# Kernel optimization log

Hardware: AMD Instinct MI355X
Metric: run time of the kernel (lower is better)

## Reference

```python
import jax, jax.numpy as jnp
import numpy as np

G, NPG, C, H, F, L = 256, 128, 16, 128, 128, 3
N = G * NPG          # 32768 nodes
E = 524288           # 16 edges per node on average
REG, REG_C = 0.01, 0.01
LN_EPS = 1e-5


def setup_inputs() -> dict:
    key = jax.random.key(0)
    ks = jax.random.split(key, 20)
    x = jax.random.normal(ks[0], (N, F), dtype=jnp.float32)
    # edges kept within each graph so dense pooling matches to_dense_batch semantics
    epg = E // G
    offs = jnp.repeat(jnp.arange(G, dtype=jnp.int64) * NPG, epg)
    src = jax.random.randint(ks[1], (E,), 0, NPG, dtype=jnp.int64) + offs
    tgt = jax.random.randint(ks[2], (E,), 0, NPG, dtype=jnp.int64) + offs
    edge_index = jnp.stack([src, tgt])
    mask_breaks = jax.random.bernoulli(ks[3], 0.5, (E,))
    s = jax.random.uniform(ks[4], (N, C), dtype=jnp.float32)
    batch = jnp.repeat(jnp.arange(G, dtype=jnp.int64), NPG)
    sc = 1.0 / np.sqrt(H)
    Wn = jax.random.normal(ks[5], (L, H, H), dtype=jnp.float32) * sc
    bn_ = jax.random.normal(ks[6], (L, H), dtype=jnp.float32) * sc
    Wo = jax.random.normal(ks[7], (L, H, H), dtype=jnp.float32) * sc
    bo = jax.random.normal(ks[8], (L, H), dtype=jnp.float32) * sc
    Wr = jax.random.normal(ks[9], (L, H, H), dtype=jnp.float32) * sc
    ln_g = jnp.ones((L, H), dtype=jnp.float32)
    ln_b = jnp.zeros((L, H), dtype=jnp.float32)
    fln_g = jnp.ones((H,), dtype=jnp.float32)
    fln_b = jnp.zeros((H,), dtype=jnp.float32)
    lin_w = jax.random.normal(ks[10], (1, H), dtype=jnp.float32) * sc
    bias = jnp.zeros((1,), dtype=jnp.float32)
    return {"x": x, "edge_index": edge_index, "mask_breaks": mask_breaks, "s": s,
            "batch": batch, "Wn": Wn, "bn_": bn_, "Wo": Wo, "bo": bo, "Wr": Wr,
            "ln_g": ln_g, "ln_b": ln_b, "fln_g": fln_g, "fln_b": fln_b,
            "lin_w": lin_w, "bias": bias}


def _layernorm(h, g, b):
    mu = jnp.mean(h, axis=-1, keepdims=True)
    v = jnp.mean(jnp.square(h - mu), axis=-1, keepdims=True)
    return (h - mu) * jax.lax.rsqrt(v + LN_EPS) * g + b


def reference(x, edge_index, mask_breaks, s, batch, Wn, bn_, Wo, bo, Wr,
              ln_g, ln_b, fln_g, fln_b, lin_w, bias):
    src, tgt = edge_index[0], edge_index[1]
    ones_e = jnp.ones((E,), dtype=x.dtype)
    cnt = jax.ops.segment_sum(ones_e, tgt, num_segments=N)          # in-degree
    inv_cnt = (1.0 / jnp.maximum(cnt, 1.0))[:, None]
    h = x
    for i in range(L):
        x_in = h @ Wn[i].T + bn_[i]
        x_out = h @ Wo[i].T + bo[i]
        x_root = h @ Wr[i].T
        msg = jnp.where(mask_breaks[:, None], x_in[src], x_out[src])  # [E,H]
        agg = jax.ops.segment_sum(msg, tgt, num_segments=N) * inv_cnt  # mean aggr
        h = jax.nn.relu(_layernorm(agg + x_root, ln_g[i], ln_b[i]))
    # dense per-graph views (equal-size graphs, batch ids sorted -> reshape)
    xd = h.reshape(G, NPG, H)
    sd = s.reshape(G, NPG, C)
    pooled = jnp.einsum("gnc,gnh->gch", sd, xd)                      # [G,C,H]
    pooled = _layernorm(pooled, fln_g, fln_b)
    xc = pooled @ lin_w.T                                            # [G,C,1]
    col_sum = sd.sum(axis=1)                                          # [G,C]
    cmask = (col_sum > 0)[..., None]
    xc = xc * cmask.astype(xc.dtype)
    out = xc.sum(axis=1) + bias                                      # [G,1]
    reg_loss = jnp.abs(Wo).sum() + jnp.abs(bo).sum()
    denom = (cmask.astype(xc.dtype).squeeze(-1) + 1e-7).sum(axis=1, keepdims=True)
    l1_loss = (jnp.abs(xc).sum(axis=1) / denom).mean()
    losses = REG * reg_loss + REG_C * l1_loss
    return out, losses, xc
```

## Files before the change

kernel.cpp:

```cpp
#include <hip/hip_runtime.h>

#define NN   32768
#define HD   128
#define EE   524288
#define GG   256
#define EPG  2048
#define CCd  16
#define LLd  3

typedef short short8 __attribute__((ext_vector_type(8)));
typedef float f32x4 __attribute__((ext_vector_type(4)));

__device__ __forceinline__ unsigned short f2bf(float f) {
  unsigned u = __builtin_bit_cast(unsigned, f);
  return (unsigned short)((u + 0x7FFFu + ((u >> 16) & 1u)) >> 16);
}
__device__ __forceinline__ unsigned bfpack(float a, float b) {
  return (unsigned)f2bf(a) | ((unsigned)f2bf(b) << 16);
}

__device__ __forceinline__ int hchunk(int f, int c) {
  return f * 128 + (((c & 8) | ((c ^ f ^ (f >> 3)) & 7)) << 3);
}
__device__ __forceinline__ int hidx(int f, int t) {
  return hchunk(f, t >> 3) + (t & 7);
}

__global__ __launch_bounds__(256) void convert_w_kernel(const float* __restrict__ Wn, const float* __restrict__ Wo,
                                                        const float* __restrict__ Wr, const float* __restrict__ bo,
                                                        unsigned* __restrict__ Wnb, unsigned* __restrict__ Wob,
                                                        unsigned* __restrict__ Wrb, float* __restrict__ wsreg) {
  int i = blockIdx.x * 256 + threadIdx.x;
  float4 a = *(const float4*)(Wn + (size_t)i * 4);
  float4 b = *(const float4*)(Wo + (size_t)i * 4);
  float4 c = *(const float4*)(Wr + (size_t)i * 4);
  *(uint2*)(Wnb + (size_t)i * 2) = make_uint2(bfpack(a.x, a.y), bfpack(a.z, a.w));
  *(uint2*)(Wob + (size_t)i * 2) = make_uint2(bfpack(b.x, b.y), bfpack(b.z, b.w));
  *(uint2*)(Wrb + (size_t)i * 2) = make_uint2(bfpack(c.x, c.y), bfpack(c.z, c.w));
  float s = fabsf(b.x) + fabsf(b.y) + fabsf(b.z) + fabsf(b.w);
  if (blockIdx.x == 0 && threadIdx.x < 96) {
    float4 d = *(const float4*)(bo + threadIdx.x * 4);
    s += fabsf(d.x) + fabsf(d.y) + fabsf(d.z) + fabsf(d.w);
  }
#pragma unroll
  for (int mk = 1; mk < 64; mk <<= 1) s += __shfl_xor(s, mk, 64);
  if ((threadIdx.x & 63) == 0) atomicAdd(wsreg, s);
}

__global__ __launch_bounds__(512) void fused_kernel(
    const float* __restrict__ x,
    const int* __restrict__ esrc, const int* __restrict__ etgt, const int* __restrict__ emask,
    const unsigned short* __restrict__ Wnb, const unsigned short* __restrict__ Wob,
    const unsigned short* __restrict__ Wrb,
    const float* __restrict__ bn, const float* __restrict__ bo,
    const float* __restrict__ lng, const float* __restrict__ lnb,
    const float* __restrict__ s,
    const float* __restrict__ flng, const float* __restrict__ flnb,
    const float* __restrict__ linw, const float* __restrict__ bias,
    float* __restrict__ out, float* __restrict__ l1g) {
  __shared__ __align__(16) unsigned short hTs[128 * 128];
  __shared__ __align__(16) unsigned short sTs[16 * 136];
  __shared__ __align__(16) unsigned Mlds[2 * 128 * 64];
  __shared__ __align__(16) unsigned Wlds[128 * 64];
  __shared__ float finS[128], foutS[128];
  __shared__ float colsumS[CCd], xcs[CCd], axcs[CCd], msk[CCd];

  const int g = blockIdx.x;
  const int tid = threadIdx.x;
  const int wave = tid >> 6;
  const int lane = tid & 63;
  const int m = lane & 15;
  const int q = lane >> 4;
  const int t0 = wave << 4;

  unsigned* const slotB = Mlds;
  unsigned* const slotC = Mlds + 8192;

  auto w_stage = [&](const unsigned short* __restrict__ Wg, unsigned* slot) {
#pragma unroll
    for (int c = 0; c < 4; ++c) {
      int row = c * 32 + wave * 4 + (lane >> 4);
      int lc = (lane & 15) ^ (row & 7);
      const unsigned short* gp = Wg + row * 128 + lc * 8;
      unsigned* lp = slot + c * 2048 + wave * 256;
      __builtin_amdgcn_global_load_lds(
          (const __attribute__((address_space(1))) unsigned*)gp,
          (__attribute__((address_space(3))) unsigned*)lp, 16, 0, 0);
    }
  };
  auto wfrag = [&](const unsigned* slot, int ct, int ksg) -> short8 {
    return *(const short8*)&slot[(ct * 16 + m) * 64 + (((ksg * 4 + q) ^ (m & 7)) << 2)];
  };

  w_stage(Wnb, Wlds);
  int et[4], es[4], em[4];
  {
    const int e0 = g * EPG;
#pragma unroll
    for (int i = 0; i < 4; ++i) {
      int e = e0 + i * 512 + tid;
      et[i] = etgt[e]; es[i] = esrc[e]; em[i] = emask[e];
    }
  }

  {
    uint4* cz = (uint4*)Mlds;
#pragma unroll
    for (int i = 0; i < 8; ++i) cz[i * 512 + tid] = make_uint4(0u, 0u, 0u, 0u);

    const float4* xg = (const float4*)(x + (size_t)g * 16384);
#pragma unroll
    for (int i = 0; i < 8; ++i) {
      int flat = i * 512 + tid;
      int t = flat >> 5, f0 = (flat & 31) << 2;
      float4 v = xg[flat];
      hTs[hidx(f0 + 0, t)] = f2bf(v.x);
      hTs[hidx(f0 + 1, t)] = f2bf(v.y);
      hTs[hidx(f0 + 2, t)] = f2bf(v.z);
      hTs[hidx(f0 + 3, t)] = f2bf(v.w);
    }
    {
      int t = tid >> 2, c0 = (tid & 3) << 2;
      float4 v = *(const float4*)(s + (size_t)g * 2048 + t * 16 + c0);
      sTs[(c0 + 0) * 136 + t] = f2bf(v.x);
      sTs[(c0 + 1) * 136 + t] = f2bf(v.y);
      sTs[(c0 + 2) * 136 + t] = f2bf(v.z);
      sTs[(c0 + 3) * 136 + t] = f2bf(v.w);
    }
    if (tid < 64) {
      int c = tid & 15, qq = tid >> 4;
      float cs = 0.f;
      for (int tt = qq; tt < 128; tt += 4) cs += s[(size_t)g * 2048 + tt * 16 + c];
      cs += __shfl_xor(cs, 16); cs += __shfl_xor(cs, 32);
      if (qq == 0) colsumS[c] = cs;
    }
  }
  __syncthreads();

  {
#pragma unroll
    for (int i = 0; i < 4; ++i) {
      int t = et[i] & 127;
      int sl = es[i] & 127;
      int dir = (em[i] != 0) ? 0 : 1;
      atomicAdd(&Mlds[dir * 8192 + t * 64 + (((sl >> 3) ^ (t & 7)) << 2) + ((sl >> 1) & 3)],
                1u << ((sl & 1) * 16));
    }
  }
  __syncthreads();

  short8 mfr[2][4];
  {
    const int t = t0 + m;
    const int mm = m & 7;
    unsigned nin = 0, nout = 0;
#pragma unroll
    for (int k4 = 0; k4 < 4; ++k4) {
      int sl = (((q * 4 + k4) ^ mm) & 15) << 2;
      uint4 a = *(const uint4*)&Mlds[t * 64 + sl];
      uint4 b = *(const uint4*)&Mlds[8192 + t * 64 + sl];
      nin  += (a.x & 0xffffu) + (a.x >> 16) + (a.y & 0xffffu) + (a.y >> 16)
            + (a.z & 0xffffu) + (a.z >> 16) + (a.w & 0xffffu) + (a.w >> 16);
      nout += (b.x & 0xffffu) + (b.x >> 16) + (b.y & 0xffffu) + (b.y >> 16)
            + (b.z & 0xffffu) + (b.z >> 16) + (b.w & 0xffffu) + (b.w >> 16);
    }
    nin  += __shfl_xor((int)nin, 16);  nin  += __shfl_xor((int)nin, 32);
    nout += __shfl_xor((int)nout, 16); nout += __shfl_xor((int)nout, 32);
    unsigned dg = nin + nout;
    float inv = 1.0f / (float)(dg > 0 ? dg : 1);
    if (q == 0) { finS[t] = (float)nin * inv; foutS[t] = (float)nout * inv; }
#pragma unroll
    for (int d = 0; d < 2; ++d)
#pragma unroll
      for (int ksg = 0; ksg < 4; ++ksg) {
        int sl = (((ksg * 4 + q) ^ mm) & 15) << 2;
        uint4 v = *(const uint4*)&Mlds[d * 8192 + t * 64 + sl];
        uint4 o;
        o.x = bfpack((float)(v.x & 0xffffu) * inv, (float)(v.x >> 16) * inv);
        o.y = bfpack((float)(v.y & 0xffffu) * inv, (float)(v.y >> 16) * inv);
        o.z = bfpack((float)(v.z & 0xffffu) * inv, (float)(v.z >> 16) * inv);
        o.w = bfpack((float)(v.w & 0xffffu) * inv, (float)(v.w >> 16) * inv);
        mfr[d][ksg] = __builtin_bit_cast(short8, o);
      }
  }
  __syncthreads();

  w_stage(Wob, slotB);
  w_stage(Wrb, slotC);
  __syncthreads();

  for (int L = 0; L < LLd; ++L) {
    const bool more = (L < LLd - 1);
    f32x4 pre[8];
#pragma unroll
    for (int ct = 0; ct < 8; ++ct) pre[ct] = (f32x4){0.f, 0.f, 0.f, 0.f};

#pragma unroll
    for (int sg = 0; sg < 2; ++sg) {
      const unsigned* slot = (sg == 0) ? (const unsigned*)Wlds : (const unsigned*)slotB;
#pragma unroll
      for (int kso = 0; kso < 4; ++kso) {
        f32x4 acc0 = (f32x4){0.f, 0.f, 0.f, 0.f};
        f32x4 acc1 = (f32x4){0.f, 0.f, 0.f, 0.f};
#pragma unroll
        for (int ksi = 0; ksi < 4; ++ksi) {
          short8 bfr = mfr[sg][ksi];
          short8 a0 = *(const short8*)&hTs[hchunk((2 * kso) * 16 + m, ksi * 4 + q)];
          acc0 = __builtin_amdgcn_mfma_f32_16x16x32_bf16(a0, bfr, acc0, 0, 0, 0);
          short8 a1 = *(const short8*)&hTs[hchunk((2 * kso + 1) * 16 + m, ksi * 4 + q)];
          acc1 = __builtin_amdgcn_mfma_f32_16x16x32_bf16(a1, bfr, acc1, 0, 0, 0);
        }
        unsigned pk[4];
#pragma unroll
        for (int r = 0; r < 4; ++r) pk[r] = bfpack(acc0[r], acc1[r]);
        short8 afr;
#pragma unroll
        for (int j = 0; j < 8; ++j) {
          int srcl = ((((q & 1) << 1) + (j >> 2)) << 4) + m;
          unsigned v = (unsigned)__shfl((int)pk[j & 3], srcl, 64);
          afr[j] = (short)(unsigned short)((q >> 1) ? (v >> 16) : (v & 0xffffu));
        }
#pragma unroll
        for (int ct = 0; ct < 8; ++ct) {
          short8 bfr = wfrag(slot, ct, kso);
          pre[ct] = __builtin_amdgcn_mfma_f32_16x16x32_bf16(afr, bfr, pre[ct], 0, 0, 0);
        }
      }
    }
#pragma unroll
    for (int hf = 0; hf < 2; ++hf)
#pragma unroll
      for (int ksl = 0; ksl < 2; ++ksl) {
        const int ksg = hf * 2 + ksl;
        short8 afr;
#pragma unroll
        for (int j = 0; j < 8; ++j)
          afr[j] = (short)hTs[hidx(ksg * 32 + q * 8 + j, t0 + m)];
#pragma unroll
        for (int ct = 0; ct < 8; ++ct) {
          short8 bfr = wfrag(slotC, ct, ksg);
          pre[ct] = __builtin_amdgcn_mfma_f32_16x16x32_bf16(afr, bfr, pre[ct], 0, 0, 0);
        }
      }
    __syncthreads();
    if (more) {
      w_stage(Wnb + (L + 1) * 16384, Wlds);
      w_stage(Wob + (L + 1) * 16384, slotB);
      w_stage(Wrb + (L + 1) * 16384, slotC);
    }
    {
      float fiv[4], fov[4];
#pragma unroll
      for (int r = 0; r < 4; ++r) { fiv[r] = finS[t0 + q * 4 + r]; fov[r] = foutS[t0 + q * 4 + r]; }
#pragma unroll
      for (int ct2 = 0; ct2 < 8; ct2 += 4) {
        float bn4[4], bo4[4];
#pragma unroll
        for (int cc = 0; cc < 4; ++cc) {
          int c = L * 128 + (ct2 + cc) * 16 + m;
          bn4[cc] = bn[c]; bo4[cc] = bo[c];
        }
#pragma unroll
        for (int cc = 0; cc < 4; ++cc)
#pragma unroll
          for (int r = 0; r < 4; ++r)
            pre[ct2 + cc][r] += fiv[r] * bn4[cc] + fov[r] * bo4[cc];
      }
      float gv[8], bv[8];
#pragma unroll
      for (int ct = 0; ct < 8; ++ct) {
        int c = L * 128 + ct * 16 + m;
        gv[ct] = lng[c]; bv[ct] = lnb[c];
      }
#pragma unroll
      for (int r = 0; r < 4; ++r) {
        const int tl = q * 4 + r;
        float sum = 0.f;
#pragma unroll
        for (int ct = 0; ct < 8; ++ct) sum += pre[ct][r];
        sum += __shfl_xor(sum, 1); sum += __shfl_xor(sum, 2);
        sum += __shfl_xor(sum, 4); sum += __shfl_xor(sum, 8);
        const float mu = sum * (1.0f / 128.0f);
        float sq = 0.f;
#pragma unroll
        for (int ct = 0; ct < 8; ++ct) { float d = pre[ct][r] - mu; sq += d * d; }
        sq += __shfl_xor(sq, 1); sq += __shfl_xor(sq, 2);
        sq += __shfl_xor(sq, 4); sq += __shfl_xor(sq, 8);
        const float rstd = rsqrtf(sq * (1.0f / 128.0f) + 1e-5f);
#pragma unroll
        for (int ct = 0; ct < 8; ++ct) {
          float o = fmaxf((pre[ct][r] - mu) * rstd * gv[ct] + bv[ct], 0.0f);
          hTs[hidx(ct * 16 + m, t0 + tl)] = f2bf(o);
        }
      }
    }
    __syncthreads();
  }

  f32x4 pl = (f32x4){0.f, 0.f, 0.f, 0.f};
#pragma unroll
  for (int ks = 0; ks < 4; ++ks) {
    short8 a = *(const short8*)&sTs[m * 136 + ks * 32 + q * 8];
    short8 b = *(const short8*)&hTs[hchunk(wave * 16 + m, ks * 4 + q)];
    pl = __builtin_amdgcn_mfma_f32_16x16x32_bf16(a, b, pl, 0, 0, 0);
  }
  float* pooledS = (float*)Mlds;
#pragma unroll
  for (int r = 0; r < 4; ++r) pooledS[(q * 4 + r) * 132 + wave * 16 + m] = pl[r];
  __syncthreads();

  if (tid < 256) {
    const int c = tid >> 4;
    const int j0 = (tid & 15) << 3;
    float v[8];
#pragma unroll
    for (int jj = 0; jj < 8; ++jj) v[jj] = pooledS[c * 132 + j0 + jj];
    float sum = 0.f;
#pragma unroll
    for (int jj = 0; jj < 8; ++jj) sum += v[jj];
#pragma unroll
    for (int mk = 1; mk < 16; mk <<= 1) sum += __shfl_xor(sum, mk, 64);
    float mu = sum * (1.0f / 128.0f);
    float sq = 0.f;
#pragma unroll
    for (int jj = 0; jj < 8; ++jj) { float d = v[jj] - mu; sq += d * d; }
#pragma unroll
    for (int mk = 1; mk < 16; mk <<= 1) sq += __shfl_xor(sq, mk, 64);
    float rstd = rsqrtf(sq * (1.0f / 128.0f) + 1e-5f);
    float dot = 0.f;
#pragma unroll
    for (int jj = 0; jj < 8; ++jj) {
      float nv = (v[jj] - mu) * rstd * flng[j0 + jj] + flnb[j0 + jj];
      dot += nv * linw[j0 + jj];
    }
#pragma unroll
    for (int mk = 1; mk < 16; mk <<= 1) dot += __shfl_xor(dot, mk, 64);
    if ((tid & 15) == 0) {
      float cm = (colsumS[c] > 0.f) ? 1.0f : 0.0f;
      float xcv = dot * cm;
      out[257 + g * CCd + c] = xcv;
      xcs[c] = xcv; axcs[c] = fabsf(xcv); msk[c] = cm;
    }
  }
  __syncthreads();
  if (tid == 0) {
    float so = 0.f, sa = 0.f, sd = 0.f;
#pragma unroll
    for (int k = 0; k < CCd; ++k) { so += xcs[k]; sa += axcs[k]; sd += msk[k] + 1e-7f; }
    out[g] = so + bias[0];
    l1g[g] = sa / sd;
  }
}

__global__ __launch_bounds__(256) void combine_kernel(const float* __restrict__ l1g, const float* __restrict__ wsreg,
                                                      float* __restrict__ outp) {
  const int tid = threadIdx.x;
  float s2 = l1g[tid];
#pragma unroll
  for (int mk = 1; mk < 64; mk <<= 1) s2 += __shfl_xor(s2, mk, 64);
  __shared__ float rs2[4];
  if ((tid & 63) == 0) rs2[tid >> 6] = s2;
  __syncthreads();
  if (tid == 0) {
    float l1 = (rs2[0] + rs2[1] + rs2[2] + rs2[3]) * (1.0f / GG);
    outp[0] = 0.01f * wsreg[0] + 0.01f * l1;
  }
}

extern "C" void kernel_launch(void* const* d_in, const int* in_sizes, int n_in,
                              void* d_out, int out_size, void* d_ws, size_t ws_size,
                              hipStream_t stream) {
  (void)in_sizes; (void)n_in; (void)out_size; (void)ws_size;
  const float* x    = (const float*)d_in[0];
  const int*   ei   = (const int*)d_in[1];
  const int*   mask = (const int*)d_in[2];
  const float* s    = (const float*)d_in[3];
  const float* Wn   = (const float*)d_in[5];
  const float* bn   = (const float*)d_in[6];
  const float* Wo   = (const float*)d_in[7];
  const float* bo   = (const float*)d_in[8];
  const float* Wr   = (const float*)d_in[9];
  const float* lng  = (const float*)d_in[10];
  const float* lnb  = (const float*)d_in[11];
  const float* flng = (const float*)d_in[12];
  const float* flnb = (const float*)d_in[13];
  const float* linw = (const float*)d_in[14];
  const float* bias = (const float*)d_in[15];
  float* out = (float*)d_out;

  char* ws = (char*)d_ws;
  size_t off = 0;
  auto alloc = [&](size_t b) { char* p = ws + off; off += (b + 255) & ~(size_t)255; return p; };
  unsigned short* Wnb = (unsigned short*)alloc((size_t)LLd * HD * HD * 2);
  unsigned short* Wob = (unsigned short*)alloc((size_t)LLd * HD * HD * 2);
  unsigned short* Wrb = (unsigned short*)alloc((size_t)LLd * HD * HD * 2);
  float* l1g    = (float*)alloc((size_t)GG * 4);
  float* wsreg  = (float*)alloc(256);

  const int* srcA = ei;
  const int* tgtA = ei + EE;

  hipMemsetAsync(wsreg, 0, 4, stream);
  convert_w_kernel<<<LLd * HD * HD / (256 * 4), 256, 0, stream>>>(Wn, Wo, Wr, bo,
      (unsigned*)Wnb, (unsigned*)Wob, (unsigned*)Wrb, wsreg);
  fused_kernel<<<GG, 512, 0, stream>>>(x, srcA, tgtA, mask, Wnb, Wob, Wrb, bn, bo,
                                       lng, lnb, s, flng, flnb, linw, bias, out, l1g);
  combine_kernel<<<1, 256, 0, stream>>>(l1g, wsreg, out + 256);
}
```

Measured before the change: 160.7 us.

## Stream weight matrices through a single LDS slot and keep adjacency in LDS

Writes the normalized bf16 adjacency back into LDS instead of holding it as register fragments. A single weight buffer in LDS is reused, with Wn, Wo and Wr loaded one after another inside each layer. The aggregation loop is restructured to compute all eight feature tiles at once per adjacency slice. This cuts register and LDS pressure, which could raise occupancy, but it adds several __syncthreads and serialises the weight loads with the MFMA work instead of prefetching them.

```diff
diff --git a/kernel.cpp b/kernel.cpp
--- a/kernel.cpp
+++ b/kernel.cpp
@@ -73,26 +73,23 @@
   const int q = lane >> 4;
   const int t0 = wave << 4;
 
-  unsigned* const slotB = Mlds;
-  unsigned* const slotC = Mlds + 8192;
-
-  auto w_stage = [&](const unsigned short* __restrict__ Wg, unsigned* slot) {
+  auto w_stage = [&](const unsigned short* __restrict__ Wg) {
 #pragma unroll
     for (int c = 0; c < 4; ++c) {
       int row = c * 32 + wave * 4 + (lane >> 4);
       int lc = (lane & 15) ^ (row & 7);
       const unsigned short* gp = Wg + row * 128 + lc * 8;
-      unsigned* lp = slot + c * 2048 + wave * 256;
+      unsigned* lp = Wlds + c * 2048 + wave * 256;
       __builtin_amdgcn_global_load_lds(
           (const __attribute__((address_space(1))) unsigned*)gp,
           (__attribute__((address_space(3))) unsigned*)lp, 16, 0, 0);
     }
   };
-  auto wfrag = [&](const unsigned* slot, int ct, int ksg) -> short8 {
-    return *(const short8*)&slot[(ct * 16 + m) * 64 + (((ksg * 4 + q) ^ (m & 7)) << 2)];
+  auto wfrag = [&](int ct, int ksg) -> short8 {
+    return *(const short8*)&Wlds[(ct * 16 + m) * 64 + (((ksg * 4 + q) ^ (m & 7)) << 2)];
   };
 
-  w_stage(Wnb, Wlds);
+  w_stage(Wnb);
   int et[4], es[4], em[4];
   {
     const int e0 = g * EPG;
@@ -149,7 +146,6 @@
   }
   __syncthreads();
 
-  short8 mfr[2][4];
   {
     const int t = t0 + m;
     const int mm = m & 7;
@@ -172,21 +168,18 @@
 #pragma unroll
     for (int d = 0; d < 2; ++d)
 #pragma unroll
-      for (int ksg = 0; ksg < 4; ++ksg) {
-        int sl = (((ksg * 4 + q) ^ mm) & 15) << 2;
-        uint4 v = *(const uint4*)&Mlds[d * 8192 + t * 64 + sl];
+      for (int k4 = 0; k4 < 4; ++k4) {
+        int sl = (((q * 4 + k4) ^ mm) & 15) << 2;
+        unsigned* p = &Mlds[d * 8192 + t * 64 + sl];
+        uint4 v = *(const uint4*)p;
         uint4 o;
         o.x = bfpack((float)(v.x & 0xffffu) * inv, (float)(v.x >> 16) * inv);
         o.y = bfpack((float)(v.y & 0xffffu) * inv, (float)(v.y >> 16) * inv);
         o.z = bfpack((float)(v.z & 0xffffu) * inv, (float)(v.z >> 16) * inv);
         o.w = bfpack((float)(v.w & 0xffffu) * inv, (float)(v.w >> 16) * inv);
-        mfr[d][ksg] = __builtin_bit_cast(short8, o);
-      }
-  }
-  __syncthreads();
-
-  w_stage(Wob, slotB);
-  w_stage(Wrb, slotC);
+        *(uint4*)p = o;
+      }
+  }
   __syncthreads();
 
   for (int L = 0; L < LLd; ++L) {
@@ -194,60 +187,91 @@
     f32x4 pre[8];
 #pragma unroll
     for (int ct = 0; ct < 8; ++ct) pre[ct] = (f32x4){0.f, 0.f, 0.f, 0.f};
-
-#pragma unroll
-    for (int sg = 0; sg < 2; ++sg) {
-      const unsigned* slot = (sg == 0) ? (const unsigned*)Wlds : (const unsigned*)slotB;
-#pragma unroll
-      for (int kso = 0; kso < 4; ++kso) {
-        f32x4 acc0 = (f32x4){0.f, 0.f, 0.f, 0.f};
-        f32x4 acc1 = (f32x4){0.f, 0.f, 0.f, 0.f};
-#pragma unroll
-        for (int ksi = 0; ksi < 4; ++ksi) {
-          short8 bfr = mfr[sg][ksi];
-          short8 a0 = *(const short8*)&hTs[hchunk((2 * kso) * 16 + m, ksi * 4 + q)];
-          acc0 = __builtin_amdgcn_mfma_f32_16x16x32_bf16(a0, bfr, acc0, 0, 0, 0);
-          short8 a1 = *(const short8*)&hTs[hchunk((2 * kso + 1) * 16 + m, ksi * 4 + q)];
-          acc1 = __builtin_amdgcn_mfma_f32_16x16x32_bf16(a1, bfr, acc1, 0, 0, 0);
-        }
-        unsigned pk[4];
-#pragma unroll
-        for (int r = 0; r < 4; ++r) pk[r] = bfpack(acc0[r], acc1[r]);
-        short8 afr;
-#pragma unroll
-        for (int j = 0; j < 8; ++j) {
-          int srcl = ((((q & 1) << 1) + (j >> 2)) << 4) + m;
-          unsigned v = (unsigned)__shfl((int)pk[j & 3], srcl, 64);
-          afr[j] = (short)(unsigned short)((q >> 1) ? (v >> 16) : (v & 0xffffu));
-        }
-#pragma unroll
-        for (int ct = 0; ct < 8; ++ct) {
-          short8 bfr = wfrag(slot, ct, kso);
-          pre[ct] = __builtin_amdgcn_mfma_f32_16x16x32_bf16(afr, bfr, pre[ct], 0, 0, 0);
-        }
-      }
-    }
-#pragma unroll
-    for (int hf = 0; hf < 2; ++hf)
-#pragma unroll
-      for (int ksl = 0; ksl < 2; ++ksl) {
-        const int ksg = hf * 2 + ksl;
-        short8 afr;
-#pragma unroll
-        for (int j = 0; j < 8; ++j)
-          afr[j] = (short)hTs[hidx(ksg * 32 + q * 8 + j, t0 + m)];
-#pragma unroll
-        for (int ct = 0; ct < 8; ++ct) {
-          short8 bfr = wfrag(slotC, ct, ksg);
-          pre[ct] = __builtin_amdgcn_mfma_f32_16x16x32_bf16(afr, bfr, pre[ct], 0, 0, 0);
-        }
-      }
-    __syncthreads();
-    if (more) {
-      w_stage(Wnb + (L + 1) * 16384, Wlds);
-      w_stage(Wob + (L + 1) * 16384, slotB);
-      w_stage(Wrb + (L + 1) * 16384, slotC);
-    }
+    f32x4 accT[8];
+
+#pragma unroll
+    for (int ft = 0; ft < 8; ++ft) accT[ft] = (f32x4){0.f, 0.f, 0.f, 0.f};
+#pragma unroll
+    for (int ksg = 0; ksg < 4; ++ksg) {
+      short8 bfr = *(const short8*)&Mlds[(t0 + m) * 64 + (((ksg * 4 + q) ^ (m & 7)) << 2)];
+#pragma unroll
+      for (int ft = 0; ft < 8; ++ft) {
+        short8 afr = *(const short8*)&hTs[hchunk(ft * 16 + m, ksg * 4 + q)];
+        accT[ft] = __builtin_amdgcn_mfma_f32_16x16x32_bf16(afr, bfr, accT[ft], 0, 0, 0);
+      }
+    }
+#pragma unroll
+    for (int ksg = 0; ksg < 4; ++ksg) {
+      f32x4 lo = accT[2 * ksg], hi = accT[2 * ksg + 1];
+      unsigned pk[4];
+#pragma unroll
+      for (int r = 0; r < 4; ++r) pk[r] = bfpack(lo[r], hi[r]);
+      short8 afr;
+#pragma unroll
+      for (int j = 0; j < 8; ++j) {
+        int srcl = ((((q & 1) << 1) + (j >> 2)) << 4) + m;
+        unsigned v = (unsigned)__shfl((int)pk[j & 3], srcl, 64);
+        afr[j] = (short)(unsigned short)((q >> 1) ? (v >> 16) : (v & 0xffffu));
+      }
+#pragma unroll
+      for (int ct = 0; ct < 8; ++ct)
+        pre[ct] = __builtin_amdgcn_mfma_f32_16x16x32_bf16(afr, wfrag(ct, ksg), pre[ct], 0, 0, 0);
+    }
+    __syncthreads();
+    w_stage(Wob + L * 16384);
+
+#pragma unroll
+    for (int ft = 0; ft < 8; ++ft) accT[ft] = (f32x4){0.f, 0.f, 0.f, 0.f};
+#pragma unroll
+    for (int ksg = 0; ksg < 4; ++ksg) {
+      short8 bfr = *(const short8*)&Mlds[8192 + (t0 + m) * 64 + (((ksg * 4 + q) ^ (m & 7)) << 2)];
+#pragma unroll
+      for (int ft = 0; ft < 8; ++ft) {
+        short8 afr = *(const short8*)&hTs[hchunk(ft * 16 + m, ksg * 4 + q)];
+        accT[ft] = __builtin_amdgcn_mfma_f32_16x16x32_bf16(afr, bfr, accT[ft], 0, 0, 0);
+      }
+    }
+    __syncthreads();
+#pragma unroll
+    for (int ksg = 0; ksg < 4; ++ksg) {
+      f32x4 lo = accT[2 * ksg], hi = accT[2 * ksg + 1];
+      unsigned pk[4];
+#pragma unroll
+      for (int r = 0; r < 4; ++r) pk[r] = bfpack(lo[r], hi[r]);
+      short8 afr;
+#pragma unroll
+      for (int j = 0; j < 8; ++j) {
+        int srcl = ((((q & 1) << 1) + (j >> 2)) << 4) + m;
+        unsigned v = (unsigned)__shfl((int)pk[j & 3], srcl, 64);
+        afr[j] = (short)(unsigned short)((q >> 1) ? (v >> 16) : (v & 0xffffu));
+      }
+#pragma unroll
+      for (int ct = 0; ct < 8; ++ct)
+        pre[ct] = __builtin_amdgcn_mfma_f32_16x16x32_bf16(afr, wfrag(ct, ksg), pre[ct], 0, 0, 0);
+    }
+    __syncthreads();
+    w_stage(Wrb + L * 16384);
+    short8 wra0, wra1, wra2, wra3;
+    {
+#pragma unroll
+      for (int j = 0; j < 8; ++j) {
+        wra0[j] = (short)hTs[hidx(0 * 32 + q * 8 + j, t0 + m)];
+        wra1[j] = (short)hTs[hidx(1 * 32 + q * 8 + j, t0 + m)];
+        wra2[j] = (short)hTs[hidx(2 * 32 + q * 8 + j, t0 + m)];
+        wra3[j] = (short)hTs[hidx(3 * 32 + q * 8 + j, t0 + m)];
+      }
+    }
+    __syncthreads();
+#pragma unroll
+    for (int ct = 0; ct < 8; ++ct) {
+      pre[ct] = __builtin_amdgcn_mfma_f32_16x16x32_bf16(wra0, wfrag(ct, 0), pre[ct], 0, 0, 0);
+      pre[ct] = __builtin_amdgcn_mfma_f32_16x16x32_bf16(wra1, wfrag(ct, 1), pre[ct], 0, 0, 0);
+      pre[ct] = __builtin_amdgcn_mfma_f32_16x16x32_bf16(wra2, wfrag(ct, 2), pre[ct], 0, 0, 0);
+      pre[ct] = __builtin_amdgcn_mfma_f32_16x16x32_bf16(wra3, wfrag(ct, 3), pre[ct], 0, 0, 0);
+    }
+    __syncthreads();
+    if (more) w_stage(Wnb + (L + 1) * 16384);
+
     {
       float fiv[4], fov[4];
 #pragma unroll
```

New measurement: 138.7 us. 1.16x faster.
